# Performance work log

Hardware: AMD Instinct MI355X
Metric: run time of the kernel (lower is better)

Reference implementation:

```python
import jax, jax.numpy as jnp
import numpy as np

FP, DP, K, S, B, T, H, ZD = 96, 28, 3, 4, 64, 8, 512, 2
CP = FP - DP + 1          # 69, valid cross-correlation output size
NP = CP * CP              # 4761 = num_pixels


def setup_inputs() -> dict:
    key = jax.random.key(0)
    ks = jax.random.split(key, 12)
    def rn(k, shape, s=0.02):
        return jax.random.normal(k, shape, jnp.float32) * s
    return {
        "frames": jax.random.uniform(ks[0], (S, B, T, FP, FP), jnp.float32),
        "conv_kernel": jax.random.uniform(ks[1], (S, B, K, DP, DP), jnp.float32),
        "eps": jax.random.normal(ks[2], (S, B, K, ZD), jnp.float32),
        "W1": rn(ks[3], (NP, H)), "b1": jnp.zeros((H,), jnp.float32),
        "Wm1": rn(ks[4], (H, H // 2)), "bm1": jnp.zeros((H // 2,), jnp.float32),
        "Wm2": rn(ks[5], (H // 2, ZD)), "bm2": jnp.zeros((ZD,), jnp.float32),
        "Ws1": rn(ks[6], (H, H // 2)), "bs1": jnp.zeros((H // 2,), jnp.float32),
        "Ws2": rn(ks[7], (H // 2, ZD)), "bs2": jnp.zeros((ZD,), jnp.float32),
        "timestep": 0,
    }


def _axis_weights(p, n):
    """Bilinear 1-D gather indices/weights with zero padding outside [0, n)."""
    p0 = jnp.floor(p)
    f = p - p0
    i0 = p0.astype(jnp.int32)
    i1 = i0 + 1
    w0 = jnp.where((i0 >= 0) & (i0 < n), 1.0 - f, 0.0)
    w1 = jnp.where((i1 >= 0) & (i1 < n), f, 0.0)
    return jnp.clip(i0, 0, n - 1), jnp.clip(i1, 0, n - 1), w0, w1


def _place_digit(digit, zw):
    """AT.digit_to_frame: place DPxDP digit into FPxFP frame at z_where (torch
    affine_grid/grid_sample, align_corners=False, zero padding). theta scale =
    FP/DP, translation = -z_where*FP/DP, i.e. in_coord = (FP/DP)*(out - zw)."""
    scale = FP / DP
    out_c = (2.0 * jnp.arange(FP, dtype=jnp.float32) + 1.0) / FP - 1.0  # (FP,)
    px = ((scale * (out_c - zw[0]) + 1.0) * DP - 1.0) * 0.5  # x source pix
    py = ((scale * (out_c - zw[1]) + 1.0) * DP - 1.0) * 0.5  # y source pix
    y0, y1, wy0, wy1 = _axis_weights(py, DP)
    x0, x1, wx0, wx1 = _axis_weights(px, DP)
    # separable bilinear: interp rows then cols
    tmp = wy0[:, None] * digit[y0, :] + wy1[:, None] * digit[y1, :]  # (FP,DP)
    return wx0[None, :] * tmp[:, x0] + wx1[None, :] * tmp[:, x1]     # (FP,FP)

_place_batch = jax.vmap(_place_digit)


def reference(frames, conv_kernel, eps, W1, b1, Wm1, bm1, Wm2, bm2,
              Ws1, bs1, Ws2, bs2, timestep):
    SB = S * B
    frame_left = frames[:, :, timestep]  # (S,B,FP,FP)
    means, stds, zs = [], [], []
    for k in range(K):
        # per-sample dynamic-kernel cross-correlation via grouped conv
        lhs = frame_left.reshape(1, SB, FP, FP)
        rhs = conv_kernel[:, :, k].reshape(SB, 1, DP, DP)
        conved = jax.lax.conv_general_dilated(
            lhs, rhs, (1, 1), 'VALID', feature_group_count=SB)  # (1,SB,CP,CP)
        scores = jax.nn.softmax(conved.reshape(S, B, NP), axis=-1)
        h = jax.nn.relu(scores @ W1 + b1)                       # (S,B,H)
        mean_k = jnp.tanh(jax.nn.relu(h @ Wm1 + bm1) @ Wm2 + bm2)
        std_k = jnp.exp(jax.nn.relu(h @ Ws1 + bs1) @ Ws2 + bs2)
        z_k = mean_k + std_k * eps[:, :, k]                     # rsample
        recon = _place_batch(conv_kernel[:, :, k].reshape(SB, DP, DP),
                             z_k.reshape(SB, ZD)).reshape(S, B, FP, FP)
        frame_left = frame_left - recon
        means.append(mean_k); stds.append(std_k); zs.append(z_k)
    q_mean = jnp.stack(means, 2)    # (S,B,K,2)
    q_std = jnp.stack(stds, 2)
    z_where = jnp.stack(zs, 2)
    return jnp.stack([q_mean, q_std, z_where], 0)  # (3,S,B,K,2)
```

## Files before the change

### kernel.cpp

```cpp
#include <hip/hip_runtime.h>
#include <hip/hip_bf16.h>
#include <math.h>

#define FPD 96
#define DPD 28
#define CPD 69
#define NPD 4761
#define KKC 3
#define SBN 256
#define TT 8
#define HD 512
#define ZDD 2
#define KPAD 4768
#define SPLITK 15
#define FRS 100
#define CVS 72

typedef __attribute__((ext_vector_type(8))) short bf16x8;
typedef __attribute__((ext_vector_type(4))) float f32x4;

__device__ __forceinline__ float bf2f_lo(unsigned int u) {
    union { unsigned int i; float f; } v; v.i = u << 16; return v.f;
}
__device__ __forceinline__ float bf2f_hi(unsigned int u) {
    union { unsigned int i; float f; } v; v.i = u & 0xffff0000u; return v.f;
}

__global__ __launch_bounds__(256) void wprep_kernel(
    const float* __restrict__ W1, const float* __restrict__ Wm1,
    const float* __restrict__ Ws1,
    ushort* __restrict__ W1T, ushort* __restrict__ WhidT)
{
    __shared__ ushort tile[64][65];
    const int t = threadIdx.x;
    const int ln = t & 63;
    const int lr = t >> 6;
    const int b = blockIdx.x;

    if (b < 600) {
        const int k0 = (b % 75) * 64;
        const int n0 = (b / 75) * 64;
        #pragma unroll
        for (int i = 0; i < 16; ++i) {
            int kk = k0 + lr + i * 4;
            float v = (kk < NPD) ? W1[(size_t)kk * HD + n0 + ln] : 0.f;
            __hip_bfloat16 h = __float2bfloat16(v);
            tile[lr + i * 4][ln] = *reinterpret_cast<ushort*>(&h);
        }
        __syncthreads();
        #pragma unroll
        for (int i = 0; i < 16; ++i) {
            int nn = lr + i * 4;
            int kk = k0 + ln;
            if (kk < KPAD)
                W1T[(size_t)(n0 + nn) * KPAD + kk] = tile[ln][nn];
        }
    } else {
        const int bb = b - 600;
        const int i0 = (bb & 7) * 64;
        const int r0 = (bb >> 3) * 64;
        #pragma unroll
        for (int rep = 0; rep < 16; ++rep) {
            int i = i0 + lr + rep * 4;
            int r = r0 + ln;
            const float* src = (r >= 256) ? Ws1 : Wm1;
            float v = src[(size_t)i * 256 + (r & 255)];
            __hip_bfloat16 h = __float2bfloat16(v);
            tile[lr + rep * 4][ln] = *reinterpret_cast<ushort*>(&h);
        }
        __syncthreads();
        #pragma unroll
        for (int rep = 0; rep < 16; ++rep) {
            int r = r0 + lr + rep * 4;
            WhidT[(size_t)r * 512 + i0 + ln] = tile[ln][lr + rep * 4];
        }
    }
}

__global__ __launch_bounds__(1024, 4) void conv_softmax_kernel(
    const float* __restrict__ frames, const int* __restrict__ tsp,
    float* __restrict__ frameL, const float* __restrict__ ck,
    const float* __restrict__ z_cur,
    ushort* __restrict__ e_buf, float* __restrict__ inv_denom, int k)
{
    __shared__ __align__(16) float fr[96 * FRS];
    __shared__ __align__(16) float kr[784];
    __shared__ float dg[784];
    __shared__ __align__(16) float cv[4][69 * CVS];
    __shared__ float red[32];

    const int t = threadIdx.x;
    const int ib = blockIdx.x;

    if (t < 784) {
        kr[t] = ck[((size_t)ib * KKC + k) * 784 + t];
        if (k > 0) dg[t] = ck[((size_t)ib * KKC + (k - 1)) * 784 + t];
    }
    float zx = 0.f, zy = 0.f;
    if (k > 0) { zx = z_cur[ib * 2]; zy = z_cur[ib * 2 + 1]; }
    __syncthreads();

    const float* src = (k < 2)
        ? frames + ((size_t)ib * TT + *tsp) * 9216
        : frameL + (size_t)ib * 9216;
    const float scale = 96.f / 28.f;
    for (int p = t; p < 9216; p += 1024) {
        int r = p / 96, c = p - r * 96;
        float val = src[p];
        if (k > 0) {
            float oci = (2.f * r + 1.f) / 96.f - 1.f;
            float ocj = (2.f * c + 1.f) / 96.f - 1.f;
            float py = ((scale * (oci - zy) + 1.f) * 28.f - 1.f) * 0.5f;
            float px = ((scale * (ocj - zx) + 1.f) * 28.f - 1.f) * 0.5f;
            float py0f = floorf(py), px0f = floorf(px);
            float fy = py - py0f, fx = px - px0f;
            int y0 = (int)py0f, x0 = (int)px0f;
            int y1 = y0 + 1, x1 = x0 + 1;
            float wy0 = (y0 >= 0 && y0 < DPD) ? 1.f - fy : 0.f;
            float wy1 = (y1 >= 0 && y1 < DPD) ? fy : 0.f;
            float wx0 = (x0 >= 0 && x0 < DPD) ? 1.f - fx : 0.f;
            float wx1 = (x1 >= 0 && x1 < DPD) ? fx : 0.f;
            int y0c = min(max(y0, 0), DPD - 1), y1c = min(max(y1, 0), DPD - 1);
            int x0c = min(max(x0, 0), DPD - 1), x1c = min(max(x1, 0), DPD - 1);
            float tmp0 = wy0 * dg[y0c * DPD + x0c] + wy1 * dg[y1c * DPD + x0c];
            float tmp1 = wy0 * dg[y0c * DPD + x1c] + wy1 * dg[y1c * DPD + x1c];
            val -= wx0 * tmp0 + wx1 * tmp1;
        }
        fr[r * FRS + c] = val;
        if (k == 1) frameL[(size_t)ib * 9216 + p] = val;
    }
    if (t < 384) fr[(t >> 2) * FRS + 96 + (t & 3)] = 0.f;
    __syncthreads();

    if (t < 828) {
        const int q    = t / 207;
        const int rem  = t - q * 207;
        const int oy   = rem / 3;
        const int tile = rem - oy * 3;
        const int ox0  = tile * 24;
        const int dy0  = q * 7;

        float acc[24];
        #pragma unroll
        for (int j = 0; j < 24; ++j) acc[j] = 0.f;

        #pragma unroll 1
        for (int dd = 0; dd < 7; ++dd) {
            const int dy = dy0 + dd;
            const float* frow = &fr[(oy + dy) * FRS + ox0];
            const float* krow = &kr[dy * 28];
            float w[52];
            #pragma unroll
            for (int u = 0; u < 13; ++u) {
                float4 v = *(const float4*)(frow + 4 * u);
                w[4*u] = v.x; w[4*u+1] = v.y; w[4*u+2] = v.z; w[4*u+3] = v.w;
            }
            #pragma unroll
            for (int d = 0; d < 28; d += 4) {
                float4 kv = *(const float4*)(krow + d);
                #pragma unroll
                for (int j = 0; j < 24; ++j) {
                    acc[j] = fmaf(w[d + j],     kv.x, acc[j]);
                    acc[j] = fmaf(w[d + j + 1], kv.y, acc[j]);
                    acc[j] = fmaf(w[d + j + 2], kv.z, acc[j]);
                    acc[j] = fmaf(w[d + j + 3], kv.w, acc[j]);
                }
            }
        }
        float* cvq = &cv[q][oy * CVS + ox0];
        #pragma unroll
        for (int u = 0; u < 6; ++u) {
            float4 v = make_float4(acc[4*u], acc[4*u+1], acc[4*u+2], acc[4*u+3]);
            *(float4*)(cvq + 4 * u) = v;
        }
    }
    __syncthreads();

    float m = -INFINITY;
    for (int p = t; p < 69 * CVS; p += 1024) {
        int ox = p - (p / CVS) * CVS;
        if (ox < CPD) {
            float v = cv[0][p] + cv[1][p] + cv[2][p] + cv[3][p];
            cv[0][p] = v;
            m = fmaxf(m, v);
        }
    }
    #pragma unroll
    for (int off = 32; off > 0; off >>= 1) m = fmaxf(m, __shfl_down(m, off, 64));
    int lane = t & 63, wid = t >> 6;
    if (lane == 0) red[wid] = m;
    __syncthreads();
    m = red[0];
    #pragma unroll
    for (int i = 1; i < 16; ++i) m = fmaxf(m, red[i]);

    float s = 0.f;
    ushort* eo = e_buf + (size_t)ib * KPAD;
    for (int p = t; p < 69 * CVS; p += 1024) {
        int oy = p / CVS;
        int ox = p - oy * CVS;
        if (ox < CPD) {
            float ev = __expf(cv[0][p] - m);
            __hip_bfloat16 h = __float2bfloat16(ev);
            eo[oy * CPD + ox] = *reinterpret_cast<ushort*>(&h);
            s += ev;
        }
    }
    #pragma unroll
    for (int off = 32; off > 0; off >>= 1) s += __shfl_down(s, off, 64);
    if (lane == 0) red[16 + wid] = s;
    __syncthreads();
    if (t == 0) {
        float tot = 0.f;
        #pragma unroll
        for (int i = 0; i < 16; ++i) tot += red[16 + i];
        inv_denom[ib] = 1.0f / tot;
    }
    if (t < KPAD - NPD) eo[NPD + t] = 0;
}

__global__ __launch_bounds__(256) void gemm1_mfma(
    const ushort* __restrict__ E, const ushort* __restrict__ W1T,
    float* __restrict__ Cpart)
{
    __shared__ __align__(16) ushort As[64][56];
    __shared__ __align__(16) ushort Bs[64][56];

    const int t  = threadIdx.x;
    const int m0 = blockIdx.x * 64;
    const int n0 = blockIdx.y * 64;
    const int z  = blockIdx.z;
    const int step0 = z * 10;
    const int nstep = min(10, 149 - step0);

    const int r = t >> 2;
    const int c = t & 3;
    const int l = t & 63;
    const int w = t >> 6;
    const int lm = l & 15;
    const int kb = l >> 4;

    f32x4 zero = {0.f, 0.f, 0.f, 0.f};
    f32x4 acc[4] = {zero, zero, zero, zero};

    const ushort* eA = E   + (size_t)(m0 + r) * KPAD + c * 8;
    const ushort* eB = W1T + (size_t)(n0 + r) * KPAD + c * 8;

    int k0 = step0 * 32;
    float4 av = *(const float4*)(eA + k0);
    float4 bv = *(const float4*)(eB + k0);

    for (int s = 0; s < nstep; ++s) {
        *(float4*)&As[r][c * 8] = av;
        *(float4*)&Bs[r][c * 8] = bv;
        __syncthreads();
        if (s + 1 < nstep) {
            int kn = (step0 + s + 1) * 32;
            av = *(const float4*)(eA + kn);
            bv = *(const float4*)(eB + kn);
        }
        bf16x8 a = *(const bf16x8*)&As[w * 16 + lm][kb * 8];
        #pragma unroll
        for (int j = 0; j < 4; ++j) {
            bf16x8 b = *(const bf16x8*)&Bs[j * 16 + lm][kb * 8];
            acc[j] = __builtin_amdgcn_mfma_f32_16x16x32_bf16(a, b, acc[j], 0, 0, 0);
        }
        __syncthreads();
    }

    const int mrow = m0 + w * 16 + kb * 4;
    #pragma unroll
    for (int j = 0; j < 4; ++j) {
        int n = n0 + j * 16 + lm;
        #pragma unroll
        for (int rg = 0; rg < 4; ++rg)
            Cpart[((size_t)z * SBN + mrow + rg) * HD + n] = acc[j][rg];
    }
}

__global__ __launch_bounds__(512) void mlp_fused(
    const float* __restrict__ Cpart, const float* __restrict__ inv_denom,
    const float* __restrict__ b1, const ushort* __restrict__ WhidT,
    const float* __restrict__ bm1, const float* __restrict__ bs1,
    const float* __restrict__ Wm2, const float* __restrict__ bm2,
    const float* __restrict__ Ws2, const float* __restrict__ bs2,
    const float* __restrict__ eps, float* __restrict__ out,
    float* __restrict__ z_cur, int k)
{
    __shared__ float hsh[HD];
    __shared__ float h2[2][256];
    __shared__ float res_sh[2][2];

    const int t = threadIdx.x;
    const int ib = blockIdx.x;

    {
        float s = 0.f;
        #pragma unroll
        for (int z = 0; z < SPLITK; ++z)
            s += Cpart[((size_t)z * SBN + ib) * HD + t];
        hsh[t] = fmaxf(fmaf(s, inv_denom[ib], b1[t]), 0.f);
    }
    __syncthreads();

    {
        int head = t >> 8, col = t & 255;
        const uint4* Wr = (const uint4*)(WhidT + (size_t)(head * 256 + col) * 512);
        float bias = head ? bs1[col] : bm1[col];
        float a = 0.f;
        #pragma unroll 8
        for (int u = 0; u < 64; ++u) {
            uint4 wv = Wr[u];
            const float* hp = &hsh[u * 8];
            a = fmaf(hp[0], bf2f_lo(wv.x), a);
            a = fmaf(hp[1], bf2f_hi(wv.x), a);
            a = fmaf(hp[2], bf2f_lo(wv.y), a);
            a = fmaf(hp[3], bf2f_hi(wv.y), a);
            a = fmaf(hp[4], bf2f_lo(wv.z), a);
            a = fmaf(hp[5], bf2f_hi(wv.z), a);
            a = fmaf(hp[6], bf2f_lo(wv.w), a);
            a = fmaf(hp[7], bf2f_hi(wv.w), a);
        }
        h2[head][col] = fmaxf(a + bias, 0.f);
    }
    __syncthreads();

    {
        int w = t >> 6, l = t & 63;
        if (w < 4) {
            int zd = (w >> 1) & 1, head = w & 1;
            const float* W2 = head ? Ws2 : Wm2;
            float a = 0.f;
            #pragma unroll
            for (int u = 0; u < 4; ++u) {
                int i = l + u * 64;
                a = fmaf(h2[head][i], W2[i * 2 + zd], a);
            }
            #pragma unroll
            for (int off = 32; off > 0; off >>= 1) a += __shfl_down(a, off, 64);
            if (l == 0) {
                float r = head ? __expf(a + bs2[zd]) : tanhf(a + bm2[zd]);
                res_sh[zd][head] = r;
            }
        }
    }
    __syncthreads();
    if (t < 2) {
        int zd = t;
        float mean = res_sh[zd][0];
        float stdv = res_sh[zd][1];
        float ev = eps[(size_t)ib * 6 + k * 2 + zd];
        float z = fmaf(stdv, ev, mean);
        int oidx = ib * 6 + k * 2 + zd;
        out[oidx]        = mean;
        out[1536 + oidx] = stdv;
        out[3072 + oidx] = z;
        z_cur[ib * 2 + zd] = z;
    }
}

extern "C" void kernel_launch(void* const* d_in, const int* in_sizes, int n_in,
                              void* d_out, int out_size, void* d_ws, size_t ws_size,
                              hipStream_t stream)
{
    const float* frames = (const float*)d_in[0];
    const float* ck     = (const float*)d_in[1];
    const float* eps    = (const float*)d_in[2];
    const float* W1     = (const float*)d_in[3];
    const float* b1     = (const float*)d_in[4];
    const float* Wm1    = (const float*)d_in[5];
    const float* bm1    = (const float*)d_in[6];
    const float* Wm2    = (const float*)d_in[7];
    const float* bm2    = (const float*)d_in[8];
    const float* Ws1    = (const float*)d_in[9];
    const float* bs1    = (const float*)d_in[10];
    const float* Ws2    = (const float*)d_in[11];
    const float* bs2    = (const float*)d_in[12];
    const int*   tsp    = (const int*)d_in[13];
    float* out = (float*)d_out;

    float* frameL  = (float*)d_ws;
    float* Cpart   = frameL + 2359296;
    float* inv_den = Cpart + 1966080;
    float* z_cur   = inv_den + 256;
    ushort* e_buf  = (ushort*)(z_cur + 512);
    ushort* W1T    = e_buf + (size_t)SBN * KPAD;
    ushort* WhidT  = W1T + (size_t)HD * KPAD;

    wprep_kernel<<<664, 256, 0, stream>>>(W1, Wm1, Ws1, W1T, WhidT);

    for (int k = 0; k < KKC; ++k) {
        conv_softmax_kernel<<<256, 1024, 0, stream>>>(
            frames, tsp, frameL, ck, z_cur, e_buf, inv_den, k);
        gemm1_mfma<<<dim3(4, 8, SPLITK), 256, 0, stream>>>(e_buf, W1T, Cpart);
        mlp_fused<<<256, 512, 0, stream>>>(Cpart, inv_den, b1, WhidT,
                                           bm1, bs1, Wm2, bm2, Ws2, bs2,
                                           eps, out, z_cur, k);
    }
}
```

Baseline: 313.5 us.

## Compute dynamic-kernel cross-correlation in fp16 with packed fdot2 instructions

Stores the frame and the per-sample kernel in shared memory as fp16 instead of fp32. The inner convolution loop now uses packed half2 dot-product instructions with fp32 accumulation, halving the number of multiply-adds and the LDS traffic per output. Odd output positions use a shifted word built by bit-splicing adjacent halves. The thread-to-tile mapping and the padded strides also change, presumably to ease LDS bank conflicts. The risk is lost precision in the conv scores that feed the softmax.

```diff
diff --git a/kernel.cpp b/kernel.cpp
--- a/kernel.cpp
+++ b/kernel.cpp
@@ -13,17 +13,22 @@
 #define ZDD 2
 #define KPAD 4768
 #define SPLITK 15
-#define FRS 100
-#define CVS 72
+#define FRSH 104
+#define CVS 76
 
 typedef __attribute__((ext_vector_type(8))) short bf16x8;
 typedef __attribute__((ext_vector_type(4))) float f32x4;
+typedef _Float16 half_t;
+typedef __attribute__((ext_vector_type(2))) _Float16 half2_t;
 
 __device__ __forceinline__ float bf2f_lo(unsigned int u) {
     union { unsigned int i; float f; } v; v.i = u << 16; return v.f;
 }
 __device__ __forceinline__ float bf2f_hi(unsigned int u) {
     union { unsigned int i; float f; } v; v.i = u & 0xffff0000u; return v.f;
+}
+__device__ __forceinline__ half2_t u2h(unsigned int u) {
+    union { unsigned int i; half2_t h; } v; v.i = u; return v.h;
 }
 
 __global__ __launch_bounds__(256) void wprep_kernel(
@@ -83,8 +88,8 @@
     const float* __restrict__ z_cur,
     ushort* __restrict__ e_buf, float* __restrict__ inv_denom, int k)
 {
-    __shared__ __align__(16) float fr[96 * FRS];
-    __shared__ __align__(16) float kr[784];
+    __shared__ __align__(16) half_t fr[96 * FRSH];
+    __shared__ __align__(16) half_t kr[28 * 32];
     __shared__ float dg[784];
     __shared__ __align__(16) float cv[4][69 * CVS];
     __shared__ float red[32];
@@ -92,10 +97,12 @@
     const int t = threadIdx.x;
     const int ib = blockIdx.x;
 
-    if (t < 784) {
-        kr[t] = ck[((size_t)ib * KKC + k) * 784 + t];
-        if (k > 0) dg[t] = ck[((size_t)ib * KKC + (k - 1)) * 784 + t];
-    }
+    if (t < 28 * 32) {
+        int dy = t >> 5, dx = t & 31;
+        float v = (dx < 28) ? ck[((size_t)ib * KKC + k) * 784 + dy * 28 + dx] : 0.f;
+        kr[t] = (half_t)v;
+    }
+    if (k > 0 && t < 784) dg[t] = ck[((size_t)ib * KKC + (k - 1)) * 784 + t];
     float zx = 0.f, zy = 0.f;
     if (k > 0) { zx = z_cur[ib * 2]; zy = z_cur[ib * 2 + 1]; }
     __syncthreads();
@@ -126,17 +133,17 @@
             float tmp1 = wy0 * dg[y0c * DPD + x1c] + wy1 * dg[y1c * DPD + x1c];
             val -= wx0 * tmp0 + wx1 * tmp1;
         }
-        fr[r * FRS + c] = val;
+        fr[r * FRSH + c] = (half_t)val;
         if (k == 1) frameL[(size_t)ib * 9216 + p] = val;
     }
-    if (t < 384) fr[(t >> 2) * FRS + 96 + (t & 3)] = 0.f;
+    if (t < 96 * 8) fr[(t >> 3) * FRSH + 96 + (t & 7)] = (half_t)0.f;
     __syncthreads();
 
     if (t < 828) {
         const int q    = t / 207;
         const int rem  = t - q * 207;
-        const int oy   = rem / 3;
-        const int tile = rem - oy * 3;
+        const int tile = rem / 69;
+        const int oy   = rem - tile * 69;
         const int ox0  = tile * 24;
         const int dy0  = q * 7;
 
@@ -147,24 +154,31 @@
         #pragma unroll 1
         for (int dd = 0; dd < 7; ++dd) {
             const int dy = dy0 + dd;
-            const float* frow = &fr[(oy + dy) * FRS + ox0];
-            const float* krow = &kr[dy * 28];
-            float w[52];
-            #pragma unroll
-            for (int u = 0; u < 13; ++u) {
-                float4 v = *(const float4*)(frow + 4 * u);
-                w[4*u] = v.x; w[4*u+1] = v.y; w[4*u+2] = v.z; w[4*u+3] = v.w;
+            const unsigned int* frow = (const unsigned int*)&fr[(oy + dy) * FRSH + ox0];
+            const unsigned int* krow = (const unsigned int*)&kr[dy * 32];
+            unsigned int W[28], K[16], V[25];
+            #pragma unroll
+            for (int u = 0; u < 7; ++u) {
+                uint4 v = *(const uint4*)(frow + 4 * u);
+                W[4*u] = v.x; W[4*u+1] = v.y; W[4*u+2] = v.z; W[4*u+3] = v.w;
             }
             #pragma unroll
-            for (int d = 0; d < 28; d += 4) {
-                float4 kv = *(const float4*)(krow + d);
+            for (int u = 0; u < 4; ++u) {
+                uint4 v = *(const uint4*)(krow + 4 * u);
+                K[4*u] = v.x; K[4*u+1] = v.y; K[4*u+2] = v.z; K[4*u+3] = v.w;
+            }
+            #pragma unroll
+            for (int i = 0; i < 25; ++i)
+                V[i] = (W[i] >> 16) | (W[i + 1] << 16);
+            #pragma unroll
+            for (int m = 0; m < 12; ++m) {
+                float ae = acc[2*m], ao = acc[2*m+1];
                 #pragma unroll
-                for (int j = 0; j < 24; ++j) {
-                    acc[j] = fmaf(w[d + j],     kv.x, acc[j]);
-                    acc[j] = fmaf(w[d + j + 1], kv.y, acc[j]);
-                    acc[j] = fmaf(w[d + j + 2], kv.z, acc[j]);
-                    acc[j] = fmaf(w[d + j + 3], kv.w, acc[j]);
+                for (int i = 0; i < 14; ++i) {
+                    ae = __builtin_amdgcn_fdot2(u2h(W[m + i]), u2h(K[i]), ae, false);
+                    ao = __builtin_amdgcn_fdot2(u2h(V[m + i]), u2h(K[i]), ao, false);
                 }
+                acc[2*m] = ae; acc[2*m+1] = ao;
             }
         }
         float* cvq = &cv[q][oy * CVS + ox0];
```

New measurement: 301.3 us. 3.9% less time.
